# Kernel tuning notes

Measured on AMD Instinct MI355X. Metric: run time of the kernel, lower is better.

Reference implementation:

```python
import jax, jax.numpy as jnp
import numpy as np

B, C_IN, L = 256, 4, 2048
HNODE, GLEN = 256, 24
SIGMA_CONV, SIGMA_NEU = 0.1, 0.1
DROPPROB = 0.5


def setup_inputs() -> dict:
    key = jax.random.key(0)
    ks = jax.random.split(key, 7)
    x = jax.random.normal(ks[0], (B, C_IN, L), dtype=jnp.float32)
    wConv = SIGMA_CONV * jax.random.normal(ks[1], (HNODE, C_IN, GLEN), dtype=jnp.float32)
    wRect = -jax.random.normal(ks[2], (HNODE,), dtype=jnp.float32)
    wHidden = 0.3 * jax.random.normal(ks[3], (2 * HNODE, 2 * HNODE), dtype=jnp.float32)
    wHiddenBias = 0.3 * jax.random.normal(ks[4], (2 * HNODE,), dtype=jnp.float32)
    wNeu = SIGMA_NEU * jax.random.normal(ks[5], (2 * HNODE, 1), dtype=jnp.float32)
    wNeuBias = SIGMA_NEU * jax.random.normal(ks[6], (1,), dtype=jnp.float32)
    return {"x": x, "wConv": wConv, "wRect": wRect, "wHidden": wHidden,
            "wHiddenBias": wHiddenBias, "wNeu": wNeu, "wNeuBias": wNeuBias}


def reference(x, wConv, wRect, wHidden, wHiddenBias, wNeu, wNeuBias):
    # conv1d, stride 1, no padding: [B, HNODE, L-GLEN+1]
    conv = jax.lax.conv_general_dilated(
        x, wConv, window_strides=(1,), padding='VALID',
        dimension_numbers=('NCH', 'OIH', 'NCH'))
    rect = jnp.maximum(conv + wRect[None, :, None], 0.0)  # bias + relu-clamp
    maxPool = jnp.max(rect, axis=2)   # [B, HNODE]
    avgPool = jnp.mean(rect, axis=2)  # [B, HNODE]
    pool = jnp.concatenate([maxPool, avgPool], axis=1)  # [B, 2*HNODE]
    hid = jnp.maximum(pool @ wHidden + wHiddenBias, 0.0)
    out = DROPPROB * (hid @ wNeu) + wNeuBias  # [B, 1]
    return out
```

## Files before the change

kernel.cpp:

```cpp
#include <hip/hip_runtime.h>
#include <stdint.h>

#define CIN   4
#define LEN   2048
#define HN    256
#define GL    24
#define LOUT  2025
#define XP    2080

typedef short  s16x8 __attribute__((ext_vector_type(8)));
typedef float  f32x4 __attribute__((ext_vector_type(4)));

static __device__ __forceinline__ uint16_t f2bf(float f) {
    union { float f; uint32_t u; } v; v.f = f;
    uint32_t u = v.u;
    return (uint16_t)((u + 0x7FFFu + ((u >> 16) & 1u)) >> 16);
}

__global__ __launch_bounds__(512, 2) void conv_pool_kernel(
    const float* __restrict__ x, const float* __restrict__ wConv,
    const float* __restrict__ wRect, float* __restrict__ pool)
{
    __shared__ uint16_t xs[CIN * XP];

    const int tid  = threadIdx.x;
    const int b    = blockIdx.x;
    const int lane = tid & 63;
    const int wid  = tid >> 6;
    const int n    = lane & 15;
    const int q    = lane >> 4;

    const float* xb = x + (size_t)b * (CIN * LEN);
    #pragma unroll
    for (int it = 0; it < 4; ++it) {
        int i = (tid + it * 512) * 4;
        float4 v = *(const float4*)(xb + i);
        int c = i >> 11, off = i & 2047;
        uint64_t pk =  (uint64_t)f2bf(v.x)
                    | ((uint64_t)f2bf(v.y) << 16)
                    | ((uint64_t)f2bf(v.z) << 32)
                    | ((uint64_t)f2bf(v.w) << 48);
        *(uint64_t*)&xs[c * XP + off] = pk;
    }
    if (tid < 64) {
        int c = tid >> 4, o = (tid & 15) * 2;
        *(uint32_t*)&xs[c * XP + 2048 + o] = 0u;
    }

    s16x8 bfrag[2][3];
    float negb[2];
    #pragma unroll
    for (int s = 0; s < 2; ++s) {
        int h = wid * 32 + s * 16 + n;
        negb[s] = -wRect[h];
        #pragma unroll
        for (int ks = 0; ks < 3; ++ks) {
            int jb = ks * 4 + q;
            const float* wp = wConv + h * (CIN * GL) + jb * 8;
            float4 w0 = *(const float4*)(wp);
            float4 w1 = *(const float4*)(wp + 4);
            s16x8 f;
            f[0]=(short)f2bf(w0.x); f[1]=(short)f2bf(w0.y);
            f[2]=(short)f2bf(w0.z); f[3]=(short)f2bf(w0.w);
            f[4]=(short)f2bf(w1.x); f[5]=(short)f2bf(w1.y);
            f[6]=(short)f2bf(w1.z); f[7]=(short)f2bf(w1.w);
            bfrag[s][ks] = f;
        }
    }

    int abase[3];
    #pragma unroll
    for (int ks = 0; ks < 3; ++ks) {
        int jb = ks * 4 + q;
        int c = jb / 3, g0 = (jb % 3) * 8;
        abase[ks] = c * XP + g0 + 8 * n;
    }

    __syncthreads();

    float rawmax[2] = {-1e30f, -1e30f};
    float sums[2]   = {0.f, 0.f};

    #pragma unroll 1
    for (int j = 0; j < 16; ++j) {
        f32x4 acc[8][2];
        #pragma unroll
        for (int ks = 0; ks < 3; ++ks) {
            const uint4 r0 = *(const uint4*)&xs[abase[ks] + 128 * j];
            const uint4 r1 = *(const uint4*)&xs[abase[ks] + 128 * j + 8];
            uint32_t d[8] = {r0.x, r0.y, r0.z, r0.w, r1.x, r1.y, r1.z, r1.w};
            #pragma unroll
            for (int p = 0; p < 8; ++p) {
                uint32_t f0, f1, f2, f3;
                if ((p & 1) == 0) {
                    f0 = d[p/2]; f1 = d[p/2+1]; f2 = d[p/2+2]; f3 = d[p/2+3];
                } else {
                    f0 = __builtin_amdgcn_alignbit(d[(p+1)/2],   d[(p-1)/2],   16);
                    f1 = __builtin_amdgcn_alignbit(d[(p+1)/2+1], d[(p-1)/2+1], 16);
                    f2 = __builtin_amdgcn_alignbit(d[(p+1)/2+2], d[(p-1)/2+2], 16);
                    f3 = __builtin_amdgcn_alignbit(d[(p+1)/2+3], d[(p-1)/2+3], 16);
                }
                uint4 fu = {f0, f1, f2, f3};
                s16x8 afrag = __builtin_bit_cast(s16x8, fu);
                #pragma unroll
                for (int s = 0; s < 2; ++s) {
                    f32x4 cin = (ks == 0) ? (f32x4){0.f, 0.f, 0.f, 0.f} : acc[p][s];
                    acc[p][s] = __builtin_amdgcn_mfma_f32_16x16x32_bf16(
                        afrag, bfrag[s][ks], cin, 0, 0, 0);
                }
            }
        }
        if (j < 15) {
            #pragma unroll
            for (int p = 0; p < 8; ++p)
                #pragma unroll
                for (int s = 0; s < 2; ++s)
                    #pragma unroll
                    for (int r = 0; r < 4; ++r) {
                        float t = fmaxf(acc[p][s][r], negb[s]);
                        sums[s]   += t;
                        rawmax[s]  = fmaxf(rawmax[s], t);
                    }
        } else {
            #pragma unroll
            for (int p = 0; p < 8; ++p)
                #pragma unroll
                for (int s = 0; s < 2; ++s)
                    #pragma unroll
                    for (int r = 0; r < 4; ++r) {
                        int tpos = p + 128 * 15 + 32 * q + 8 * r;
                        float t = (tpos < LOUT) ? fmaxf(acc[p][s][r], negb[s])
                                                : negb[s];
                        sums[s]   += t;
                        rawmax[s]  = fmaxf(rawmax[s], t);
                    }
        }
    }

    #pragma unroll
    for (int s = 0; s < 2; ++s) {
        float m  = rawmax[s], sm = sums[s];
        m  = fmaxf(m, __shfl_xor(m, 16, 64));  sm += __shfl_xor(sm, 16, 64);
        m  = fmaxf(m, __shfl_xor(m, 32, 64));  sm += __shfl_xor(sm, 32, 64);
        if (q == 0) {
            int h = wid * 32 + s * 16 + n;
            float bia = -negb[s];
            pool[(size_t)b * 512 + h]       = fmaxf(m + bia, 0.f);
            pool[(size_t)b * 512 + 256 + h] = (sm + 2048.f * bia) * (1.0f / 2025.0f);
        }
    }
}

__global__ __launch_bounds__(256, 4) void mlp_kernel(
    const float* __restrict__ pool, const float* __restrict__ wH,
    const float* __restrict__ bH, const float* __restrict__ wNeu,
    const float* __restrict__ wNeuB, float* __restrict__ out)
{
    __shared__ float pl[8][512];

    const int tid = threadIdx.x;
    const int og  = blockIdx.x & 7;
    const int bg  = blockIdx.x >> 3;
    const int o   = og * 64 + (tid & 63);
    const int wv  = tid >> 6;

    const float* ps = pool + (size_t)bg * 8 * 512;
    #pragma unroll
    for (int it = 0; it < 4; ++it) {
        int i = (tid + it * 256) * 4;
        *(float4*)&pl[0][i] = *(const float4*)(ps + i);
    }
    __syncthreads();

    float acc0 = 0.f, acc1 = 0.f;
    const float* prow0 = &pl[wv * 2][0];
    const float* prow1 = &pl[wv * 2 + 1][0];
    #pragma unroll 4
    for (int i = 0; i < 512; i += 4) {
        float4 p0 = *(const float4*)(prow0 + i);
        float4 p1 = *(const float4*)(prow1 + i);
        float w0 = wH[(i + 0) * 512 + o];
        float w1 = wH[(i + 1) * 512 + o];
        float w2 = wH[(i + 2) * 512 + o];
        float w3 = wH[(i + 3) * 512 + o];
        acc0 = fmaf(p0.x, w0, acc0); acc0 = fmaf(p0.y, w1, acc0);
        acc0 = fmaf(p0.z, w2, acc0); acc0 = fmaf(p0.w, w3, acc0);
        acc1 = fmaf(p1.x, w0, acc1); acc1 = fmaf(p1.y, w1, acc1);
        acc1 = fmaf(p1.z, w2, acc1); acc1 = fmaf(p1.w, w3, acc1);
    }
    float hb  = bH[o];
    float wn  = wNeu[o];
    float v0  = fmaxf(acc0 + hb, 0.f) * wn;
    float v1  = fmaxf(acc1 + hb, 0.f) * wn;
    #pragma unroll
    for (int dlt = 1; dlt < 64; dlt <<= 1) {
        v0 += __shfl_xor(v0, dlt, 64);
        v1 += __shfl_xor(v1, dlt, 64);
    }
    if ((tid & 63) == 0) {
        int b0 = bg * 8 + wv * 2;
        float bias = (og == 0) ? wNeuB[0] : 0.f;
        atomicAdd(&out[b0],     0.5f * v0 + bias);
        atomicAdd(&out[b0 + 1], 0.5f * v1 + bias);
    }
}

extern "C" void kernel_launch(void* const* d_in, const int* in_sizes, int n_in,
                              void* d_out, int out_size, void* d_ws, size_t ws_size,
                              hipStream_t stream) {
    const float* x        = (const float*)d_in[0];
    const float* wConv    = (const float*)d_in[1];
    const float* wRect    = (const float*)d_in[2];
    const float* wHidden  = (const float*)d_in[3];
    const float* wHidBias = (const float*)d_in[4];
    const float* wNeu     = (const float*)d_in[5];
    const float* wNeuBias = (const float*)d_in[6];
    float* out  = (float*)d_out;
    float* pool = (float*)d_ws;

    hipMemsetAsync(d_out, 0, 256 * sizeof(float), stream);
    conv_pool_kernel<<<256, 512, 0, stream>>>(x, wConv, wRect, pool);
    mlp_kernel<<<256, 256, 0, stream>>>(pool, wHidden, wHidBias, wNeu, wNeuBias, out);
}
```

Measured before the change: 123.9 us.

## Split conv sequence across two wave halves with 1024-thread blocks and shared-memory combine

```diff
diff --git a/kernel.cpp b/kernel.cpp
--- a/kernel.cpp
+++ b/kernel.cpp
@@ -17,23 +17,40 @@
     return (uint16_t)((u + 0x7FFFu + ((u >> 16) & 1u)) >> 16);
 }
 
-__global__ __launch_bounds__(512, 2) void conv_pool_kernel(
+#define MKFRAG(dd, p) \
+    ({ uint32_t f0_, f1_, f2_, f3_; \
+       if (((p) & 1) == 0) { \
+           f0_ = dd[(p)/2];   f1_ = dd[(p)/2+1]; \
+           f2_ = dd[(p)/2+2]; f3_ = dd[(p)/2+3]; \
+       } else { \
+           f0_ = __builtin_amdgcn_alignbit(dd[((p)+1)/2],   dd[((p)-1)/2],   16); \
+           f1_ = __builtin_amdgcn_alignbit(dd[((p)+1)/2+1], dd[((p)-1)/2+1], 16); \
+           f2_ = __builtin_amdgcn_alignbit(dd[((p)+1)/2+2], dd[((p)-1)/2+2], 16); \
+           f3_ = __builtin_amdgcn_alignbit(dd[((p)+1)/2+3], dd[((p)-1)/2+3], 16); \
+       } \
+       uint4 fu_ = {f0_, f1_, f2_, f3_}; __builtin_bit_cast(s16x8, fu_); })
+
+__global__ __launch_bounds__(1024, 4) void conv_pool_kernel(
     const float* __restrict__ x, const float* __restrict__ wConv,
     const float* __restrict__ wRect, float* __restrict__ pool)
 {
     __shared__ uint16_t xs[CIN * XP];
+    __shared__ float pmax_l[2][HN];
+    __shared__ float psum_l[2][HN];
 
     const int tid  = threadIdx.x;
     const int b    = blockIdx.x;
     const int lane = tid & 63;
     const int wid  = tid >> 6;
+    const int wp   = wid & 7;
+    const int wh   = wid >> 3;
     const int n    = lane & 15;
     const int q    = lane >> 4;
 
     const float* xb = x + (size_t)b * (CIN * LEN);
     #pragma unroll
-    for (int it = 0; it < 4; ++it) {
-        int i = (tid + it * 512) * 4;
+    for (int it = 0; it < 2; ++it) {
+        int i = (tid + it * 1024) * 4;
         float4 v = *(const float4*)(xb + i);
         int c = i >> 11, off = i & 2047;
         uint64_t pk =  (uint64_t)f2bf(v.x)
@@ -51,14 +68,14 @@
     float negb[2];
     #pragma unroll
     for (int s = 0; s < 2; ++s) {
-        int h = wid * 32 + s * 16 + n;
+        int h = wp * 32 + s * 16 + n;
         negb[s] = -wRect[h];
         #pragma unroll
         for (int ks = 0; ks < 3; ++ks) {
             int jb = ks * 4 + q;
-            const float* wp = wConv + h * (CIN * GL) + jb * 8;
-            float4 w0 = *(const float4*)(wp);
-            float4 w1 = *(const float4*)(wp + 4);
+            const float* wp_ = wConv + h * (CIN * GL) + jb * 8;
+            float4 w0 = *(const float4*)(wp_);
+            float4 w1 = *(const float4*)(wp_ + 4);
             s16x8 f;
             f[0]=(short)f2bf(w0.x); f[1]=(short)f2bf(w0.y);
             f[2]=(short)f2bf(w0.z); f[3]=(short)f2bf(w0.w);
@@ -80,60 +97,70 @@
 
     float rawmax[2] = {-1e30f, -1e30f};
     float sums[2]   = {0.f, 0.f};
+    const f32x4 fzero = {0.f, 0.f, 0.f, 0.f};
 
     #pragma unroll 1
-    for (int j = 0; j < 16; ++j) {
-        f32x4 acc[8][2];
+    for (int jj = 0; jj < 8; ++jj) {
+        const int j = wh * 8 + jj;
+        const bool tail = (j == 15);
+
+        uint32_t d0[8], d1[8], d2[8];
+        {
+            const uint4 r0 = *(const uint4*)&xs[abase[0] + 128 * j];
+            const uint4 r1 = *(const uint4*)&xs[abase[0] + 128 * j + 8];
+            d0[0]=r0.x; d0[1]=r0.y; d0[2]=r0.z; d0[3]=r0.w;
+            d0[4]=r1.x; d0[5]=r1.y; d0[6]=r1.z; d0[7]=r1.w;
+        }
+        {
+            const uint4 r0 = *(const uint4*)&xs[abase[1] + 128 * j];
+            const uint4 r1 = *(const uint4*)&xs[abase[1] + 128 * j + 8];
+            d1[0]=r0.x; d1[1]=r0.y; d1[2]=r0.z; d1[3]=r0.w;
+            d1[4]=r1.x; d1[5]=r1.y; d1[6]=r1.z; d1[7]=r1.w;
+        }
+        {
+            const uint4 r0 = *(const uint4*)&xs[abase[2] + 128 * j];
+            const uint4 r1 = *(const uint4*)&xs[abase[2] + 128 * j + 8];
+            d2[0]=r0.x; d2[1]=r0.y; d2[2]=r0.z; d2[3]=r0.w;
+            d2[4]=r1.x; d2[5]=r1.y; d2[6]=r1.z; d2[7]=r1.w;
+        }
+
         #pragma unroll
-        for (int ks = 0; ks < 3; ++ks) {
-            const uint4 r0 = *(const uint4*)&xs[abase[ks] + 128 * j];
-            const uint4 r1 = *(const uint4*)&xs[abase[ks] + 128 * j + 8];
-            uint32_t d[8] = {r0.x, r0.y, r0.z, r0.w, r1.x, r1.y, r1.z, r1.w};
-            #pragma unroll
-            for (int p = 0; p < 8; ++p) {
-                uint32_t f0, f1, f2, f3;
-                if ((p & 1) == 0) {
-                    f0 = d[p/2]; f1 = d[p/2+1]; f2 = d[p/2+2]; f3 = d[p/2+3];
-                } else {
-                    f0 = __builtin_amdgcn_alignbit(d[(p+1)/2],   d[(p-1)/2],   16);
-                    f1 = __builtin_amdgcn_alignbit(d[(p+1)/2+1], d[(p-1)/2+1], 16);
-                    f2 = __builtin_amdgcn_alignbit(d[(p+1)/2+2], d[(p-1)/2+2], 16);
-                    f3 = __builtin_amdgcn_alignbit(d[(p+1)/2+3], d[(p-1)/2+3], 16);
-                }
-                uint4 fu = {f0, f1, f2, f3};
-                s16x8 afrag = __builtin_bit_cast(s16x8, fu);
+        for (int p = 0; p < 8; ++p) {
+            s16x8 a0 = MKFRAG(d0, p);
+            s16x8 a1 = MKFRAG(d1, p);
+            s16x8 a2 = MKFRAG(d2, p);
+            f32x4 acc[2];
+            acc[0] = __builtin_amdgcn_mfma_f32_16x16x32_bf16(a0, bfrag[0][0], fzero, 0, 0, 0);
+            acc[1] = __builtin_amdgcn_mfma_f32_16x16x32_bf16(a0, bfrag[1][0], fzero, 0, 0, 0);
+            acc[0] = __builtin_amdgcn_mfma_f32_16x16x32_bf16(a1, bfrag[0][1], acc[0], 0, 0, 0);
+            acc[1] = __builtin_amdgcn_mfma_f32_16x16x32_bf16(a1, bfrag[1][1], acc[1], 0, 0, 0);
+            acc[0] = __builtin_amdgcn_mfma_f32_16x16x32_bf16(a2, bfrag[0][2], acc[0], 0, 0, 0);
+            acc[1] = __builtin_amdgcn_mfma_f32_16x16x32_bf16(a2, bfrag[1][2], acc[1], 0, 0, 0);
+
+            if (!tail) {
                 #pragma unroll
                 for (int s = 0; s < 2; ++s) {
-                    f32x4 cin = (ks == 0) ? (f32x4){0.f, 0.f, 0.f, 0.f} : acc[p][s];
-                    acc[p][s] = __builtin_amdgcn_mfma_f32_16x16x32_bf16(
-                        afrag, bfrag[s][ks], cin, 0, 0, 0);
+                    const f32x4 a = acc[s];
+                    float t0 = fmaxf(a[0], negb[s]), t1 = fmaxf(a[1], negb[s]);
+                    float t2 = fmaxf(a[2], negb[s]), t3 = fmaxf(a[3], negb[s]);
+                    sums[s] += (t0 + t1) + (t2 + t3);
+                    rawmax[s] = fmaxf(fmaxf(rawmax[s], a[0]), a[1]);
+                    rawmax[s] = fmaxf(fmaxf(rawmax[s], a[2]), a[3]);
                 }
-            }
-        }
-        if (j < 15) {
-            #pragma unroll
-            for (int p = 0; p < 8; ++p)
+            } else {
                 #pragma unroll
-                for (int s = 0; s < 2; ++s)
-                    #pragma unroll
-                    for (int r = 0; r < 4; ++r) {
-                        float t = fmaxf(acc[p][s][r], negb[s]);
-                        sums[s]   += t;
-                        rawmax[s]  = fmaxf(rawmax[s], t);
-                    }
-        } else {
-            #pragma unroll
-            for (int p = 0; p < 8; ++p)
-                #pragma unroll
-                for (int s = 0; s < 2; ++s)
+                for (int s = 0; s < 2; ++s) {
+                    const f32x4 a = acc[s];
                     #pragma unroll
                     for (int r = 0; r < 4; ++r) {
                         int tpos = p + 128 * 15 + 32 * q + 8 * r;
-                        float t = (tpos < LOUT) ? fmaxf(acc[p][s][r], negb[s])
+                        float t = (tpos < LOUT) ? fmaxf(a[r], negb[s])
                                                 : negb[s];
                         sums[s]   += t;
                         rawmax[s]  = fmaxf(rawmax[s], t);
                     }
+                }
+            }
         }
     }
 
@@ -143,11 +170,19 @@
         m  = fmaxf(m, __shfl_xor(m, 16, 64));  sm += __shfl_xor(sm, 16, 64);
         m  = fmaxf(m, __shfl_xor(m, 32, 64));  sm += __shfl_xor(sm, 32, 64);
         if (q == 0) {
-            int h = wid * 32 + s * 16 + n;
-            float bia = -negb[s];
-            pool[(size_t)b * 512 + h]       = fmaxf(m + bia, 0.f);
-            pool[(size_t)b * 512 + 256 + h] = (sm + 2048.f * bia) * (1.0f / 2025.0f);
-        }
+            int h = wp * 32 + s * 16 + n;
+            pmax_l[wh][h] = m;
+            psum_l[wh][h] = sm;
+        }
+    }
+    __syncthreads();
+
+    if (tid < HN) {
+        float m   = fmaxf(pmax_l[0][tid], pmax_l[1][tid]);
+        float sm  = psum_l[0][tid] + psum_l[1][tid];
+        float bia = wRect[tid];
+        pool[(size_t)b * 512 + tid]       = fmaxf(m + bia, 0.f);
+        pool[(size_t)b * 512 + 256 + tid] = (sm + 2048.f * bia) * (1.0f / 2025.0f);
     }
 }
 
@@ -219,6 +254,6 @@
     float* pool = (float*)d_ws;
 
     hipMemsetAsync(d_out, 0, 256 * sizeof(float), stream);
-    conv_pool_kernel<<<256, 512, 0, stream>>>(x, wConv, wRect, pool);
+    conv_pool_kernel<<<256, 1024, 0, stream>>>(x, wConv, wRect, pool);
     mlp_kernel<<<256, 256, 0, stream>>>(pool, wHidden, wHidBias, wNeu, wNeuBias, out);
 }
```

After: 125.4 us. About the same (+1.2%).

## Precompute odd-shifted input copy in LDS and double-buffer conv register windows

Applied to the files above, without the earlier changes.

```diff
diff --git a/kernel.cpp b/kernel.cpp
--- a/kernel.cpp
+++ b/kernel.cpp
@@ -11,17 +11,91 @@
 typedef short  s16x8 __attribute__((ext_vector_type(8)));
 typedef float  f32x4 __attribute__((ext_vector_type(4)));
 
+__device__ float g_pool[256 * 512];
+
 static __device__ __forceinline__ uint16_t f2bf(float f) {
     union { float f; uint32_t u; } v; v.f = f;
     uint32_t u = v.u;
     return (uint16_t)((u + 0x7FFFu + ((u >> 16) & 1u)) >> 16);
 }
 
-__global__ __launch_bounds__(512, 2) void conv_pool_kernel(
+#define SEL4(D, i) \
+    ({ uint4 fu_ = {(D)[(i)], (D)[(i)+1], (D)[(i)+2], (D)[(i)+3]}; \
+       __builtin_bit_cast(s16x8, fu_); })
+
+static __device__ __forceinline__ void loadW(
+    uint32_t (&E)[3][8], uint32_t (&O)[3][8],
+    const uint16_t* xs, const uint16_t* xs2, const int (&abase)[3], int j)
+{
+    #pragma unroll
+    for (int ks = 0; ks < 3; ++ks) {
+        const uint4 e0 = *(const uint4*)&xs [abase[ks] + 128 * j];
+        const uint4 e1 = *(const uint4*)&xs [abase[ks] + 128 * j + 8];
+        const uint4 o0 = *(const uint4*)&xs2[abase[ks] + 128 * j];
+        const uint4 o1 = *(const uint4*)&xs2[abase[ks] + 128 * j + 8];
+        E[ks][0]=e0.x; E[ks][1]=e0.y; E[ks][2]=e0.z; E[ks][3]=e0.w;
+        E[ks][4]=e1.x; E[ks][5]=e1.y; E[ks][6]=e1.z; E[ks][7]=e1.w;
+        O[ks][0]=o0.x; O[ks][1]=o0.y; O[ks][2]=o0.z; O[ks][3]=o0.w;
+        O[ks][4]=o1.x; O[ks][5]=o1.y; O[ks][6]=o1.z; O[ks][7]=o1.w;
+    }
+}
+
+static __device__ __forceinline__ void procW(
+    const uint32_t (&E)[3][8], const uint32_t (&O)[3][8],
+    const s16x8 (&bfrag)[2][3], const float (&negb)[2],
+    bool tail, int q, float (&rawmax)[2], float (&sums)[2])
+{
+    const f32x4 fzero = {0.f, 0.f, 0.f, 0.f};
+    #pragma unroll
+    for (int p = 0; p < 8; ++p) {
+        s16x8 a0, a1, a2;
+        if ((p & 1) == 0) {
+            a0 = SEL4(E[0], p/2); a1 = SEL4(E[1], p/2); a2 = SEL4(E[2], p/2);
+        } else {
+            a0 = SEL4(O[0], (p-1)/2); a1 = SEL4(O[1], (p-1)/2); a2 = SEL4(O[2], (p-1)/2);
+        }
+        f32x4 acc0, acc1;
+        acc0 = __builtin_amdgcn_mfma_f32_16x16x32_bf16(a0, bfrag[0][0], fzero, 0, 0, 0);
+        acc1 = __builtin_amdgcn_mfma_f32_16x16x32_bf16(a0, bfrag[1][0], fzero, 0, 0, 0);
+        acc0 = __builtin_amdgcn_mfma_f32_16x16x32_bf16(a1, bfrag[0][1], acc0, 0, 0, 0);
+        acc1 = __builtin_amdgcn_mfma_f32_16x16x32_bf16(a1, bfrag[1][1], acc1, 0, 0, 0);
+        acc0 = __builtin_amdgcn_mfma_f32_16x16x32_bf16(a2, bfrag[0][2], acc0, 0, 0, 0);
+        acc1 = __builtin_amdgcn_mfma_f32_16x16x32_bf16(a2, bfrag[1][2], acc1, 0, 0, 0);
+
+        if (!tail) {
+            #pragma unroll
+            for (int s = 0; s < 2; ++s) {
+                const f32x4 a = (s == 0) ? acc0 : acc1;
+                float t0 = fmaxf(a[0], negb[s]), t1 = fmaxf(a[1], negb[s]);
+                float t2 = fmaxf(a[2], negb[s]), t3 = fmaxf(a[3], negb[s]);
+                sums[s] += (t0 + t1) + (t2 + t3);
+                rawmax[s] = fmaxf(fmaxf(rawmax[s], a[0]), a[1]);
+                rawmax[s] = fmaxf(fmaxf(rawmax[s], a[2]), a[3]);
+            }
+        } else {
+            #pragma unroll
+            for (int s = 0; s < 2; ++s) {
+                const f32x4 a = (s == 0) ? acc0 : acc1;
+                #pragma unroll
+                for (int r = 0; r < 4; ++r) {
+                    int tpos = p + 128 * 15 + 32 * q + 8 * r;
+                    float t = (tpos < LOUT) ? fmaxf(a[r], negb[s])
+                                            : negb[s];
+                    sums[s]   += t;
+                    rawmax[s]  = fmaxf(rawmax[s], t);
+                }
+            }
+        }
+    }
+}
+
+__global__ __launch_bounds__(512) __attribute__((amdgpu_waves_per_eu(2, 2)))
+void conv_pool_kernel(
     const float* __restrict__ x, const float* __restrict__ wConv,
-    const float* __restrict__ wRect, float* __restrict__ pool)
-{
-    __shared__ uint16_t xs[CIN * XP];
+    const float* __restrict__ wRect)
+{
+    __shared__ uint16_t xs [CIN * XP + 8];
+    __shared__ uint16_t xs2[CIN * XP + 8];
 
     const int tid  = threadIdx.x;
     const int b    = blockIdx.x;
@@ -46,6 +120,7 @@
         int c = tid >> 4, o = (tid & 15) * 2;
         *(uint32_t*)&xs[c * XP + 2048 + o] = 0u;
     }
+    if (tid < 4) *(uint32_t*)&xs[CIN * XP + tid * 2] = 0u;
 
     s16x8 bfrag[2][3];
     float negb[2];
@@ -56,9 +131,9 @@
         #pragma unroll
         for (int ks = 0; ks < 3; ++ks) {
             int jb = ks * 4 + q;
-            const float* wp = wConv + h * (CIN * GL) + jb * 8;
-            float4 w0 = *(const float4*)(wp);
-            float4 w1 = *(const float4*)(wp + 4);
+            const float* wp_ = wConv + h * (CIN * GL) + jb * 8;
+            float4 w0 = *(const float4*)(wp_);
+            float4 w1 = *(const float4*)(wp_ + 4);
             s16x8 f;
             f[0]=(short)f2bf(w0.x); f[1]=(short)f2bf(w0.y);
             f[2]=(short)f2bf(w0.z); f[3]=(short)f2bf(w0.w);
@@ -78,63 +153,34 @@
 
     __syncthreads();
 
+    {
+        const uint32_t* s0 = (const uint32_t*)xs;
+        uint32_t*       s1 = (uint32_t*)xs2;
+        #pragma unroll 1
+        for (int g = tid; g < (CIN * XP) / 8; g += 512) {
+            uint4 a = *(const uint4*)&s0[4 * g];
+            uint32_t nx = s0[4 * g + 4];
+            uint4 r;
+            r.x = __builtin_amdgcn_alignbit(a.y, a.x, 16);
+            r.y = __builtin_amdgcn_alignbit(a.z, a.y, 16);
+            r.z = __builtin_amdgcn_alignbit(a.w, a.z, 16);
+            r.w = __builtin_amdgcn_alignbit(nx,  a.w, 16);
+            *(uint4*)&s1[4 * g] = r;
+        }
+    }
+    __syncthreads();
+
     float rawmax[2] = {-1e30f, -1e30f};
     float sums[2]   = {0.f, 0.f};
 
+    uint32_t EA[3][8], OA[3][8], EB[3][8], OB[3][8];
+    loadW(EA, OA, xs, xs2, abase, 0);
     #pragma unroll 1
-    for (int j = 0; j < 16; ++j) {
-        f32x4 acc[8][2];
-        #pragma unroll
-        for (int ks = 0; ks < 3; ++ks) {
-            const uint4 r0 = *(const uint4*)&xs[abase[ks] + 128 * j];
-            const uint4 r1 = *(const uint4*)&xs[abase[ks] + 128 * j + 8];
-            uint32_t d[8] = {r0.x, r0.y, r0.z, r0.w, r1.x, r1.y, r1.z, r1.w};
-            #pragma unroll
-            for (int p = 0; p < 8; ++p) {
-                uint32_t f0, f1, f2, f3;
-                if ((p & 1) == 0) {
-                    f0 = d[p/2]; f1 = d[p/2+1]; f2 = d[p/2+2]; f3 = d[p/2+3];
-                } else {
-                    f0 = __builtin_amdgcn_alignbit(d[(p+1)/2],   d[(p-1)/2],   16);
-                    f1 = __builtin_amdgcn_alignbit(d[(p+1)/2+1], d[(p-1)/2+1], 16);
-                    f2 = __builtin_amdgcn_alignbit(d[(p+1)/2+2], d[(p-1)/2+2], 16);
-                    f3 = __builtin_amdgcn_alignbit(d[(p+1)/2+3], d[(p-1)/2+3], 16);
-                }
-                uint4 fu = {f0, f1, f2, f3};
-                s16x8 afrag = __builtin_bit_cast(s16x8, fu);
-                #pragma unroll
-                for (int s = 0; s < 2; ++s) {
-                    f32x4 cin = (ks == 0) ? (f32x4){0.f, 0.f, 0.f, 0.f} : acc[p][s];
-                    acc[p][s] = __builtin_amdgcn_mfma_f32_16x16x32_bf16(
-                        afrag, bfrag[s][ks], cin, 0, 0, 0);
-                }
-            }
-        }
-        if (j < 15) {
-            #pragma unroll
-            for (int p = 0; p < 8; ++p)
-                #pragma unroll
-                for (int s = 0; s < 2; ++s)
-                    #pragma unroll
-                    for (int r = 0; r < 4; ++r) {
-                        float t = fmaxf(acc[p][s][r], negb[s]);
-                        sums[s]   += t;
-                        rawmax[s]  = fmaxf(rawmax[s], t);
-                    }
-        } else {
-            #pragma unroll
-            for (int p = 0; p < 8; ++p)
-                #pragma unroll
-                for (int s = 0; s < 2; ++s)
-                    #pragma unroll
-                    for (int r = 0; r < 4; ++r) {
-                        int tpos = p + 128 * 15 + 32 * q + 8 * r;
-                        float t = (tpos < LOUT) ? fmaxf(acc[p][s][r], negb[s])
-                                                : negb[s];
-                        sums[s]   += t;
-                        rawmax[s]  = fmaxf(rawmax[s], t);
-                    }
-        }
+    for (int jj = 0; jj < 16; jj += 2) {
+        loadW(EB, OB, xs, xs2, abase, jj + 1);
+        procW(EA, OA, bfrag, negb, false, q, rawmax, sums);
+        loadW(EA, OA, xs, xs2, abase, (jj + 2 < 16) ? jj + 2 : 15);
+        procW(EB, OB, bfrag, negb, (jj + 1 == 15), q, rawmax, sums);
     }
 
     #pragma unroll
@@ -145,16 +191,16 @@
         if (q == 0) {
             int h = wid * 32 + s * 16 + n;
             float bia = -negb[s];
-            pool[(size_t)b * 512 + h]       = fmaxf(m + bia, 0.f);
-            pool[(size_t)b * 512 + 256 + h] = (sm + 2048.f * bia) * (1.0f / 2025.0f);
+            g_pool[(size_t)b * 512 + h]       = fmaxf(m + bia, 0.f);
+            g_pool[(size_t)b * 512 + 256 + h] = (sm + 2048.f * bia) * (1.0f / 2025.0f);
         }
     }
 }
 
 __global__ __launch_bounds__(256, 4) void mlp_kernel(
-    const float* __restrict__ pool, const float* __restrict__ wH,
-    const float* __restrict__ bH, const float* __restrict__ wNeu,
-    const float* __restrict__ wNeuB, float* __restrict__ out)
+    const float* __restrict__ wH, const float* __restrict__ bH,
+    const float* __restrict__ wNeu, const float* __restrict__ wNeuB,
+    float* __restrict__ out)
 {
     __shared__ float pl[8][512];
 
@@ -164,7 +210,7 @@
     const int o   = og * 64 + (tid & 63);
     const int wv  = tid >> 6;
 
-    const float* ps = pool + (size_t)bg * 8 * 512;
+    const float* ps = g_pool + (size_t)bg * 8 * 512;
     #pragma unroll
     for (int it = 0; it < 4; ++it) {
         int i = (tid + it * 256) * 4;
@@ -216,9 +262,9 @@
     const float* wNeu     = (const float*)d_in[5];
     const float* wNeuBias = (const float*)d_in[6];
     float* out  = (float*)d_out;
-    float* pool = (float*)d_ws;
+    (void)d_ws; (void)ws_size;
 
     hipMemsetAsync(d_out, 0, 256 * sizeof(float), stream);
-    conv_pool_kernel<<<256, 512, 0, stream>>>(x, wConv, wRect, pool);
-    mlp_kernel<<<256, 256, 0, stream>>>(pool, wHidden, wHidBias, wNeu, wNeuBias, out);
-}
+    conv_pool_kernel<<<256, 512, 0, stream>>>(x, wConv, wRect);
+    mlp_kernel<<<256, 256, 0, stream>>>(wHidden, wHidBias, wNeu, wNeuBias, out);
+}
```

Measured after the change: 123.4 us. Within noise of the previous version (-0.4%).
